# Optimization experiments

Measured on AMD Instinct MI355X. Metric: run time of the kernel, lower is better.

The kernel has to match this reference:

```python
import jax, jax.numpy as jnp
import numpy as np

# MiniCPM3 MLA attention dims
HIDDEN = 2560
N_HEADS = 40
Q_LORA = 768
KV_LORA = 256
ROPE_D = 32
NOPE_D = 64
V_D = HIDDEN // N_HEADS          # 64
Q_HEAD_D = NOPE_D + ROPE_D       # 96
ROPE_BASE = 10000.0
EPS = 1e-6


def setup_inputs() -> dict:
    key = jax.random.key(0)
    ks = jax.random.split(key, 8)
    B, S = 1, 2048
    sc = lambda fan_in: 1.0 / np.sqrt(fan_in)
    return {
        "hidden_states": jax.random.normal(ks[0], (B, S, HIDDEN), jnp.float32),
        "position_ids": jnp.arange(B * S, dtype=jnp.int64).reshape(B, S) % S,
        "w_qa": jax.random.normal(ks[1], (HIDDEN, Q_LORA), jnp.float32) * sc(HIDDEN),
        "q_a_ln_w": jnp.ones((Q_LORA,), jnp.float32),
        "w_qb": jax.random.normal(ks[2], (Q_LORA, N_HEADS * Q_HEAD_D), jnp.float32) * sc(Q_LORA),
        "w_kva": jax.random.normal(ks[3], (HIDDEN, KV_LORA + ROPE_D), jnp.float32) * sc(HIDDEN),
        "kv_a_ln_w": jnp.ones((KV_LORA,), jnp.float32),
        "w_kvb": jax.random.normal(ks[4], (KV_LORA, N_HEADS * (NOPE_D + V_D)), jnp.float32) * sc(KV_LORA),
        "w_o": jax.random.normal(ks[5], (N_HEADS * V_D, HIDDEN), jnp.float32) * sc(N_HEADS * V_D),
    }


def _rmsnorm(x, w, eps=EPS):
    var = jnp.mean(x * x, axis=-1, keepdims=True)
    return x * jax.lax.rsqrt(var + eps) * w


def _rotate_half(x):
    h = x.shape[-1] // 2
    return jnp.concatenate([-x[..., h:], x[..., :h]], axis=-1)


def _rope_cache(seq_len, dim, base, dtype=jnp.float32):
    inv_freq = 1.0 / (base ** (jnp.arange(0, dim, 2, dtype=jnp.float32) / dim))
    t = jnp.arange(seq_len, dtype=jnp.float32)
    freqs = jnp.outer(t, inv_freq)                      # [S, dim/2]
    emb = jnp.concatenate([freqs, freqs], axis=-1)      # [S, dim]
    return jnp.cos(emb).astype(dtype), jnp.sin(emb).astype(dtype)


def reference(hidden_states, position_ids, w_qa, q_a_ln_w, w_qb, w_kva, kv_a_ln_w, w_kvb, w_o):
    B, S, _ = hidden_states.shape
    # --- low-rank Q projection: a -> RMSNorm -> b ---
    q = _rmsnorm(hidden_states @ w_qa, q_a_ln_w) @ w_qb          # [B,S,H*96]
    q = q.reshape(B, S, N_HEADS, Q_HEAD_D).transpose(0, 2, 1, 3)  # [B,H,S,96]
    q_nope, q_pe = q[..., :NOPE_D], q[..., NOPE_D:]
    # --- compressed KV + shared rope key ---
    ckv = hidden_states @ w_kva                                   # [B,S,256+32]
    compressed_kv, k_pe = ckv[..., :KV_LORA], ckv[..., KV_LORA:]
    k_pe = k_pe[:, None, :, :]                                    # [B,1,S,32]
    kv = _rmsnorm(compressed_kv, kv_a_ln_w) @ w_kvb               # [B,S,H*(64+64)]
    kv = kv.reshape(B, S, N_HEADS, NOPE_D + V_D).transpose(0, 2, 1, 3)
    k_nope, v = kv[..., :NOPE_D], kv[..., NOPE_D:]                # [B,H,S,64] each
    # --- RoPE on the 32-dim rope sub-dimension (fp32, as original) ---
    cos, sin = _rope_cache(S, ROPE_D, ROPE_BASE)
    cos = cos[position_ids][:, None, :, :]                        # [B,1,S,32]
    sin = sin[position_ids][:, None, :, :]
    q_pe = q_pe * cos + _rotate_half(q_pe) * sin
    k_pe = k_pe * cos + _rotate_half(k_pe) * sin
    # --- concat nope/rope parts ---
    q_full = jnp.concatenate([q_nope, q_pe], axis=-1)             # [B,H,S,96]
    k_full = jnp.concatenate([k_nope, jnp.broadcast_to(k_pe, (B, N_HEADS, S, ROPE_D))], axis=-1)
    # --- causal SDPA with scale q_head_dim**-0.5 ---
    scale = Q_HEAD_D ** -0.5
    scores = jnp.einsum("bhqd,bhkd->bhqk", q_full, k_full) * scale
    causal = jnp.tril(jnp.ones((S, S), bool))
    scores = jnp.where(causal, scores, jnp.finfo(scores.dtype).min)
    probs = jax.nn.softmax(scores, axis=-1)
    attn = jnp.einsum("bhqk,bhkd->bhqd", probs, v)                # [B,H,S,64]
    attn = attn.transpose(0, 2, 1, 3).reshape(B, S, N_HEADS * V_D)
    return attn @ w_o
```

## Files before the change

kernel.cpp:

```cpp
#include <hip/hip_runtime.h>
#include <hip/hip_bf16.h>

typedef __hip_bfloat16 bf16;
typedef __attribute__((ext_vector_type(8))) __bf16 bf16x8;
typedef __attribute__((ext_vector_type(4))) __bf16 bf16x4;
typedef __attribute__((ext_vector_type(4))) float f32x4;

constexpr int S_LEN = 2048;
constexpr int HID   = 2560;
constexpr int NH    = 40;
constexpr int QL    = 768;
constexpr int KVL   = 256;
constexpr int RD    = 32;
constexpr int ND    = 64;
constexpr int VD    = 64;
constexpr int QHD   = 96;
constexpr int QB_N  = NH * QHD;
constexpr int KVB_N = NH * (ND + VD);
constexpr int CKV_N = KVL + RD;
constexpr int AB_N  = QL + CKV_N;

#define MFMA16(a, b, c) __builtin_amdgcn_mfma_f32_16x16x32_bf16((a), (b), (c), 0, 0, 0)

__device__ __forceinline__ int get_pos(const int* pos, int s) {
  bool is64 = (pos[1] == 0 && pos[2] == 1);
  return is64 ? pos[2 * s] : pos[s];
}


__global__ void cast_f32_bf16(const float* __restrict__ src, bf16* __restrict__ dst, int n4) {
  int i = blockIdx.x * blockDim.x + threadIdx.x;
  if (i >= n4) return;
  float4 v = reinterpret_cast<const float4*>(src)[i];
  struct { bf16 a, b, c, d; } pk;
  pk.a = __float2bfloat16(v.x); pk.b = __float2bfloat16(v.y);
  pk.c = __float2bfloat16(v.z); pk.d = __float2bfloat16(v.w);
  reinterpret_cast<uint2*>(dst)[i] = *reinterpret_cast<uint2*>(&pk);
}

__global__ void transpose_cast(const float* __restrict__ src, bf16* __restrict__ dst, int K, int N) {
  __shared__ float tile[32][33];
  int nb = blockIdx.x * 32, kb = blockIdx.y * 32;
  int x = threadIdx.x, y = threadIdx.y;
#pragma unroll
  for (int j = 0; j < 4; ++j) {
    int k = kb + y + j * 8, n = nb + x;
    tile[y + j * 8][x] = (k < K && n < N) ? src[(size_t)k * N + n] : 0.f;
  }
  __syncthreads();
#pragma unroll
  for (int j = 0; j < 4; ++j) {
    int n = nb + y + j * 8, k = kb + x;
    if (n < N && k < K) dst[(size_t)n * K + k] = __float2bfloat16(tile[x][y + j * 8]);
  }
}


template<bool OBF16, bool NEDGE>
__global__ __launch_bounds__(256) void gemm_bt(const bf16* __restrict__ A,
                                               const bf16* __restrict__ B,
                                               void* __restrict__ Cv,
                                               int M, int N, int K) {
  constexpr int BM = 128, BN = 128, BK = 64;
  __shared__ __bf16 ldsA[BM * BK];
  __shared__ __bf16 ldsB[BN * BK];
  const int t = threadIdx.x;
  const int l = t & 63, w = t >> 6;
  const int lr = l & 15, lk = l >> 4;
  const int wr = w >> 1, wc = w & 1;
  const int rowbase = blockIdx.y * BM;
  const int colbase = blockIdx.x * BN;

  f32x4 acc[4][4];
#pragma unroll
  for (int m = 0; m < 4; ++m)
#pragma unroll
    for (int n = 0; n < 4; ++n) acc[m][n] = f32x4{0.f, 0.f, 0.f, 0.f};

  const int kiters = K / BK;
  for (int kt = 0; kt < kiters; ++kt) {
    const int kb = kt * BK;
#pragma unroll
    for (int it = 0; it < 4; ++it) {
      const int r  = it * 32 + w * 8 + (l >> 3);
      const int c8 = ((l & 7) * 8) ^ ((r & 7) << 3);
      const bf16* ga = A + (size_t)(rowbase + r) * K + kb + c8;
      __builtin_amdgcn_global_load_lds((const __attribute__((address_space(1))) void*)ga,
          (__attribute__((address_space(3))) void*)(ldsA + it * 2048 + w * 512), 16, 0, 0);
      int nrow = colbase + r;
      if (NEDGE) nrow = (nrow < N) ? nrow : (N - 1);
      const bf16* gb = B + (size_t)nrow * K + kb + c8;
      __builtin_amdgcn_global_load_lds((const __attribute__((address_space(1))) void*)gb,
          (__attribute__((address_space(3))) void*)(ldsB + it * 2048 + w * 512), 16, 0, 0);
    }
    __syncthreads();
#pragma unroll
    for (int kk = 0; kk < 2; ++kk) {
      bf16x8 af[4], bfr[4];
#pragma unroll
      for (int m = 0; m < 4; ++m) {
        const int row = wr * 64 + m * 16 + lr;
        const int ce  = (kk * 32 + lk * 8) ^ ((row & 7) << 3);
        af[m] = *(const bf16x8*)(ldsA + row * BK + ce);
      }
#pragma unroll
      for (int n = 0; n < 4; ++n) {
        const int row = wc * 64 + n * 16 + lr;
        const int ce  = (kk * 32 + lk * 8) ^ ((row & 7) << 3);
        bfr[n] = *(const bf16x8*)(ldsB + row * BK + ce);
      }
#pragma unroll
      for (int m = 0; m < 4; ++m)
#pragma unroll
        for (int n = 0; n < 4; ++n)
          acc[m][n] = MFMA16(af[m], bfr[n], acc[m][n]);
    }
    __syncthreads();
  }

#pragma unroll
  for (int m = 0; m < 4; ++m)
#pragma unroll
    for (int n = 0; n < 4; ++n) {
      const int col = colbase + wc * 64 + n * 16 + lr;
      if (NEDGE && col >= N) continue;
#pragma unroll
      for (int i = 0; i < 4; ++i) {
        const int row = rowbase + wr * 64 + m * 16 + lk * 4 + i;
        if (OBF16) ((bf16*)Cv)[(size_t)row * N + col] = __float2bfloat16(acc[m][n][i]);
        else       ((float*)Cv)[(size_t)row * N + col] = acc[m][n][i];
      }
    }
}

__global__ __launch_bounds__(256) void gemm_qakva(const bf16* __restrict__ A,
                                                  const bf16* __restrict__ B,
                                                  float* __restrict__ q_out,
                                                  float* __restrict__ ckv_out) {
  constexpr int BM = 128, BK = 64, K = HID, N = AB_N;
  __shared__ __bf16 ldsA[BM * BK];
  __shared__ __bf16 ldsB[64 * BK];
  const int t = threadIdx.x;
  const int l = t & 63, w = t >> 6;
  const int lr = l & 15, lk = l >> 4;
  const int rowbase = blockIdx.y * BM;
  const int colbase = blockIdx.x * 64;

  f32x4 acc[2][4];
#pragma unroll
  for (int m = 0; m < 2; ++m)
#pragma unroll
    for (int n = 0; n < 4; ++n) acc[m][n] = f32x4{0.f, 0.f, 0.f, 0.f};

  for (int kt = 0; kt < K / BK; ++kt) {
    const int kb = kt * BK;
#pragma unroll
    for (int it = 0; it < 4; ++it) {
      const int r  = it * 32 + w * 8 + (l >> 3);
      const int c8 = ((l & 7) * 8) ^ ((r & 7) << 3);
      const bf16* ga = A + (size_t)(rowbase + r) * K + kb + c8;
      __builtin_amdgcn_global_load_lds((const __attribute__((address_space(1))) void*)ga,
          (__attribute__((address_space(3))) void*)(ldsA + it * 2048 + w * 512), 16, 0, 0);
      if (it < 2) {
        int nrow = colbase + r;
        nrow = (nrow < N) ? nrow : (N - 1);
        const bf16* gb = B + (size_t)nrow * K + kb + c8;
        __builtin_amdgcn_global_load_lds((const __attribute__((address_space(1))) void*)gb,
            (__attribute__((address_space(3))) void*)(ldsB + it * 2048 + w * 512), 16, 0, 0);
      }
    }
    __syncthreads();
#pragma unroll
    for (int kk = 0; kk < 2; ++kk) {
      bf16x8 af[2], bfr[4];
#pragma unroll
      for (int m = 0; m < 2; ++m) {
        const int row = w * 32 + m * 16 + lr;
        const int ce  = (kk * 32 + lk * 8) ^ ((row & 7) << 3);
        af[m] = *(const bf16x8*)(ldsA + row * BK + ce);
      }
#pragma unroll
      for (int n = 0; n < 4; ++n) {
        const int row = n * 16 + lr;
        const int ce  = (kk * 32 + lk * 8) ^ ((row & 7) << 3);
        bfr[n] = *(const bf16x8*)(ldsB + row * BK + ce);
      }
#pragma unroll
      for (int m = 0; m < 2; ++m)
#pragma unroll
        for (int n = 0; n < 4; ++n)
          acc[m][n] = MFMA16(af[m], bfr[n], acc[m][n]);
    }
    __syncthreads();
  }

#pragma unroll
  for (int m = 0; m < 2; ++m)
#pragma unroll
    for (int n = 0; n < 4; ++n) {
      const int col = colbase + n * 16 + lr;
#pragma unroll
      for (int i = 0; i < 4; ++i) {
        const int row = rowbase + w * 32 + m * 16 + lk * 4 + i;
        if (col < QL)       q_out[(size_t)row * QL + col] = acc[m][n][i];
        else if (col < N)   ckv_out[(size_t)row * CKV_N + (col - QL)] = acc[m][n][i];
      }
    }
}

__global__ __launch_bounds__(256) void gemm_qb_rope(const bf16* __restrict__ A,
                                                    const bf16* __restrict__ B,
                                                    const float* __restrict__ ropc,
                                                    const float* __restrict__ rops,
                                                    bf16* __restrict__ qfull) {
  constexpr int BM = 128, BN = 128, BK = 64, K = QL, N = QB_N;
  __shared__ __bf16 ldsA[BM * BK];
  __shared__ __bf16 ldsB[BN * BK];
  const int t = threadIdx.x;
  const int l = t & 63, w = t >> 6;
  const int lr = l & 15, lk = l >> 4;
  const int wr = w >> 1, wc = w & 1;
  const int rowbase = blockIdx.y * BM;
  const int colbase = blockIdx.x * BN;
  const float scale = 0.14724444f;

  f32x4 acc[4][4];
#pragma unroll
  for (int m = 0; m < 4; ++m)
#pragma unroll
    for (int n = 0; n < 4; ++n) acc[m][n] = f32x4{0.f, 0.f, 0.f, 0.f};

  for (int kt = 0; kt < K / BK; ++kt) {
    const int kb = kt * BK;
#pragma unroll
    for (int it = 0; it < 4; ++it) {
      const int r  = it * 32 + w * 8 + (l >> 3);
      const int c8 = ((l & 7) * 8) ^ ((r & 7) << 3);
      const bf16* ga = A + (size_t)(rowbase + r) * K + kb + c8;
      __builtin_amdgcn_global_load_lds((const __attribute__((address_space(1))) void*)ga,
          (__attribute__((address_space(3))) void*)(ldsA + it * 2048 + w * 512), 16, 0, 0);
      const bf16* gb = B + (size_t)(colbase + r) * K + kb + c8;
      __builtin_amdgcn_global_load_lds((const __attribute__((address_space(1))) void*)gb,
          (__attribute__((address_space(3))) void*)(ldsB + it * 2048 + w * 512), 16, 0, 0);
    }
    __syncthreads();
#pragma unroll
    for (int kk = 0; kk < 2; ++kk) {
      bf16x8 af[4], bfr[4];
#pragma unroll
      for (int m = 0; m < 4; ++m) {
        const int row = wr * 64 + m * 16 + lr;
        const int ce  = (kk * 32 + lk * 8) ^ ((row & 7) << 3);
        af[m] = *(const bf16x8*)(ldsA + row * BK + ce);
      }
#pragma unroll
      for (int n = 0; n < 4; ++n) {
        const int row = wc * 64 + n * 16 + lr;
        const int ce  = (kk * 32 + lk * 8) ^ ((row & 7) << 3);
        bfr[n] = *(const bf16x8*)(ldsB + row * BK + ce);
      }
#pragma unroll
      for (int m = 0; m < 4; ++m)
#pragma unroll
        for (int n = 0; n < 4; ++n)
          acc[m][n] = MFMA16(af[m], bfr[n], acc[m][n]);
    }
    __syncthreads();
  }

#pragma unroll
  for (int m = 0; m < 4; ++m) {
    const int rowtop = rowbase + wr * 64 + m * 16 + lk * 4;
#pragma unroll
    for (int n = 0; n < 4; ++n) {
      const int c0 = colbase + wc * 64 + n * 16;
      const int h  = c0 / 96;
      const int d0 = c0 - h * 96;
      const size_t qb_ = ((size_t)h * S_LEN + rowtop) * QHD + d0 + lr;
      if (d0 < ND) {
#pragma unroll
        for (int i = 0; i < 4; ++i)
          qfull[qb_ + (size_t)i * QHD] = __float2bfloat16(acc[m][n][i] * scale);
      } else if (d0 == ND) {
#pragma unroll
        for (int i = 0; i < 4; ++i) {
          const float c = ropc[(rowtop + i) * 16 + lr];
          const float s = rops[(rowtop + i) * 16 + lr];
          const float x0 = acc[m][n][i], x1 = acc[m][n + 1][i];
          qfull[qb_ + (size_t)i * QHD] = __float2bfloat16((x0 * c - x1 * s) * scale);
        }
      } else {
#pragma unroll
        for (int i = 0; i < 4; ++i) {
          const float c = ropc[(rowtop + i) * 16 + lr];
          const float s = rops[(rowtop + i) * 16 + lr];
          const float x1 = acc[m][n][i], x0 = acc[m][n - 1][i];
          qfull[qb_ + (size_t)i * QHD] = __float2bfloat16((x1 * c + x0 * s) * scale);
        }
      }
    }
  }
}

__global__ __launch_bounds__(256) void gemm_kvb_split(const bf16* __restrict__ A,
                                                      const bf16* __restrict__ B,
                                                      bf16* __restrict__ knope,
                                                      bf16* __restrict__ vt) {
  constexpr int BM = 128, BN = 128, BK = 64, K = KVL;
  __shared__ __bf16 ldsA[BM * BK];
  __shared__ __bf16 ldsB[BN * BK];
  const int t = threadIdx.x;
  const int l = t & 63, w = t >> 6;
  const int lr = l & 15, lk = l >> 4;
  const int wr = w >> 1, wc = w & 1;
  const int rowbase = blockIdx.y * BM;
  const int h = blockIdx.x;
  const int colbase = h * BN;

  f32x4 acc[4][4];
#pragma unroll
  for (int m = 0; m < 4; ++m)
#pragma unroll
    for (int n = 0; n < 4; ++n) acc[m][n] = f32x4{0.f, 0.f, 0.f, 0.f};

  for (int kt = 0; kt < K / BK; ++kt) {
    const int kb = kt * BK;
#pragma unroll
    for (int it = 0; it < 4; ++it) {
      const int r  = it * 32 + w * 8 + (l >> 3);
      const int c8 = ((l & 7) * 8) ^ ((r & 7) << 3);
      const bf16* ga = A + (size_t)(rowbase + r) * K + kb + c8;
      __builtin_amdgcn_global_load_lds((const __attribute__((address_space(1))) void*)ga,
          (__attribute__((address_space(3))) void*)(ldsA + it * 2048 + w * 512), 16, 0, 0);
      const bf16* gb = B + (size_t)(colbase + r) * K + kb + c8;
      __builtin_amdgcn_global_load_lds((const __attribute__((address_space(1))) void*)gb,
          (__attribute__((address_space(3))) void*)(ldsB + it * 2048 + w * 512), 16, 0, 0);
    }
    __syncthreads();
#pragma unroll
    for (int kk = 0; kk < 2; ++kk) {
      bf16x8 af[4], bfr[4];
#pragma unroll
      for (int m = 0; m < 4; ++m) {
        const int row = wr * 64 + m * 16 + lr;
        const int ce  = (kk * 32 + lk * 8) ^ ((row & 7) << 3);
        af[m] = *(const bf16x8*)(ldsA + row * BK + ce);
      }
#pragma unroll
      for (int n = 0; n < 4; ++n) {
        const int row = wc * 64 + n * 16 + lr;
        const int ce  = (kk * 32 + lk * 8) ^ ((row & 7) << 3);
        bfr[n] = *(const bf16x8*)(ldsB + row * BK + ce);
      }
#pragma unroll
      for (int m = 0; m < 4; ++m)
#pragma unroll
        for (int n = 0; n < 4; ++n)
          acc[m][n] = MFMA16(af[m], bfr[n], acc[m][n]);
    }
    __syncthreads();
  }

#pragma unroll
  for (int m = 0; m < 4; ++m) {
    const int rowtop = rowbase + wr * 64 + m * 16 + lk * 4;
    if (wc == 0) {
#pragma unroll
      for (int n = 0; n < 4; ++n) {
        const int d = n * 16 + lr;
#pragma unroll
        for (int i = 0; i < 4; ++i)
          knope[((size_t)h * S_LEN + rowtop + i) * ND + d] = __float2bfloat16(acc[m][n][i]);
      }
    } else {
#pragma unroll
      for (int n = 0; n < 4; ++n) {
        const int d = n * 16 + lr;
        bf16x4 pk;
#pragma unroll
        for (int i = 0; i < 4; ++i) pk[i] = (__bf16)acc[m][n][i];
        *(bf16x4*)(vt + ((size_t)h * VD + d) * S_LEN + rowtop) = pk;
      }
    }
  }
}


__global__ void rmsnorm_rows(const float* __restrict__ in, const float* __restrict__ w,
                             bf16* __restrict__ out, int C) {
  const int r = blockIdx.x;
  const float* row = in + (size_t)r * C;
  float ss = 0.f;
  for (int c = threadIdx.x; c < C; c += 256) { float v = row[c]; ss += v * v; }
#pragma unroll
  for (int d = 32; d > 0; d >>= 1) ss += __shfl_xor(ss, d);
  __shared__ float red[4];
  if ((threadIdx.x & 63) == 0) red[threadIdx.x >> 6] = ss;
  __syncthreads();
  const float tot = red[0] + red[1] + red[2] + red[3];
  const float rs = rsqrtf(tot / (float)C + 1e-6f);
  for (int c = threadIdx.x; c < C; c += 256)
    out[(size_t)r * C + c] = __float2bfloat16(row[c] * rs * w[c]);
}

__global__ void kv_prep(const float* __restrict__ ckv, const float* __restrict__ w,
                        const int* __restrict__ pos, bf16* __restrict__ ckv_bf,
                        bf16* __restrict__ kpe, float* __restrict__ ropc,
                        float* __restrict__ rops) {
  const int s = blockIdx.x, t = threadIdx.x;
  const float* row = ckv + (size_t)s * CKV_N;
  float v[4]; float ss = 0.f;
#pragma unroll
  for (int j = 0; j < 4; ++j) { v[j] = row[t + 64 * j]; ss += v[j] * v[j]; }
#pragma unroll
  for (int d = 32; d > 0; d >>= 1) ss += __shfl_xor(ss, d);
  const float rs = rsqrtf(ss / (float)KVL + 1e-6f);
#pragma unroll
  for (int j = 0; j < 4; ++j)
    ckv_bf[(size_t)s * KVL + t + 64 * j] = __float2bfloat16(v[j] * rs * w[t + 64 * j]);
  if (t < 16) {
    const float x0 = row[KVL + t], x1 = row[KVL + 16 + t];
    const float p = (float)get_pos(pos, s);
    const float invf = exp2f(-(float)t * (13.2877124f / 16.f));
    const float ang = p * invf, c = cosf(ang), sn = sinf(ang);
    ropc[s * 16 + t] = c;
    rops[s * 16 + t] = sn;
    kpe[(size_t)s * RD + t]      = __float2bfloat16(x0 * c - x1 * sn);
    kpe[(size_t)s * RD + 16 + t] = __float2bfloat16(x1 * c + x0 * sn);
  }
}

__global__ __launch_bounds__(64) void attn_kernel(const bf16* __restrict__ qfull,
                                                  const bf16* __restrict__ knope,
                                                  const bf16* __restrict__ kpe,
                                                  const bf16* __restrict__ vt,
                                                  bf16* __restrict__ ctx) {
  const int h = blockIdx.x;
  const int qw = ((int)gridDim.y - 1 - (int)blockIdx.y) * 32;
  const int l = threadIdx.x;
  const int lr = l & 15, lk = l >> 4;
  const bf16* Q  = qfull + (size_t)h * S_LEN * QHD;
  const bf16* Kn = knope + (size_t)h * S_LEN * ND;
  const bf16* V  = vt + (size_t)h * VD * S_LEN;
  __shared__ __bf16 plds[32][64];

  bf16x8 qf[2][3];
#pragma unroll
  for (int qg = 0; qg < 2; ++qg)
#pragma unroll
    for (int ks = 0; ks < 3; ++ks)
      qf[qg][ks] = *(const bf16x8*)(Q + (size_t)(qw + qg * 16 + lr) * QHD + ks * 32 + lk * 8);

  f32x4 o[2][4];
  float mrow[2], lrow[2];
#pragma unroll
  for (int qg = 0; qg < 2; ++qg) {
#pragma unroll
    for (int dt = 0; dt < 4; ++dt) o[qg][dt] = f32x4{0.f, 0.f, 0.f, 0.f};
    mrow[qg] = -1e30f; lrow[qg] = 0.f;
  }

  bf16x8 kf[4][3];
#pragma unroll
  for (int sub = 0; sub < 4; ++sub) {
#pragma unroll
    for (int ks = 0; ks < 2; ++ks)
      kf[sub][ks] = *(const bf16x8*)(Kn + (size_t)(sub * 16 + lr) * ND + ks * 32 + lk * 8);
    kf[sub][2] = *(const bf16x8*)(kpe + (size_t)(sub * 16 + lr) * RD + lk * 8);
  }

  for (int kb = 0;; kb += 64) {
    f32x4 st[2][4];
#pragma unroll
    for (int qg = 0; qg < 2; ++qg)
#pragma unroll
      for (int sub = 0; sub < 4; ++sub) st[qg][sub] = f32x4{0.f, 0.f, 0.f, 0.f};
#pragma unroll
    for (int qg = 0; qg < 2; ++qg)
#pragma unroll
      for (int sub = 0; sub < 4; ++sub)
#pragma unroll
        for (int ks = 0; ks < 3; ++ks)
          st[qg][sub] = MFMA16(kf[sub][ks], qf[qg][ks], st[qg][sub]);

    const int nkb = kb + 64;
    if (nkb <= qw) {
#pragma unroll
      for (int sub = 0; sub < 4; ++sub) {
#pragma unroll
        for (int ks = 0; ks < 2; ++ks)
          kf[sub][ks] = *(const bf16x8*)(Kn + (size_t)(nkb + sub * 16 + lr) * ND + ks * 32 + lk * 8);
        kf[sub][2] = *(const bf16x8*)(kpe + (size_t)(nkb + sub * 16 + lr) * RD + lk * 8);
      }
    }

    const bool diag = (kb + 64 > qw);
    float tm[2];
#pragma unroll
    for (int qg = 0; qg < 2; ++qg) {
      const int q = qw + qg * 16 + lr;
      if (diag) {
#pragma unroll
        for (int sub = 0; sub < 4; ++sub)
#pragma unroll
          for (int i = 0; i < 4; ++i)
            if (kb + sub * 16 + lk * 4 + i > q) st[qg][sub][i] = -1e30f;
      }
      float m0 = -1e30f;
#pragma unroll
      for (int sub = 0; sub < 4; ++sub)
#pragma unroll
        for (int i = 0; i < 4; ++i) m0 = fmaxf(m0, st[qg][sub][i]);
      m0 = fmaxf(m0, __shfl_xor(m0, 16));
      m0 = fmaxf(m0, __shfl_xor(m0, 32));
      tm[qg] = m0;
    }

    const bool noresc = __all((tm[0] <= mrow[0] + 8.f) && (tm[1] <= mrow[1] + 8.f));
    float fac[2];
#pragma unroll
    for (int qg = 0; qg < 2; ++qg) {
      const float mnew = noresc ? mrow[qg] : fmaxf(mrow[qg], tm[qg]);
      float ts = 0.f;
#pragma unroll
      for (int sub = 0; sub < 4; ++sub) {
        bf16x4 pk;
#pragma unroll
        for (int i = 0; i < 4; ++i) {
          const float p = exp2f(st[qg][sub][i] - mnew);
          ts += p;
          pk[i] = (__bf16)p;
        }
        const int swc = (sub * 16 + lk * 4) ^ ((lr & 7) << 3);
        *(bf16x4*)(&plds[qg * 16 + lr][swc]) = pk;
      }
      ts += __shfl_xor(ts, 16);
      ts += __shfl_xor(ts, 32);
      if (noresc) {
        lrow[qg] += ts;
      } else {
        fac[qg] = exp2f(mrow[qg] - mnew);
        lrow[qg] = lrow[qg] * fac[qg] + ts;
        mrow[qg] = mnew;
      }
    }
    if (!noresc) {
#pragma unroll
      for (int qg = 0; qg < 2; ++qg)
#pragma unroll
        for (int i = 0; i < 4; ++i) {
          const float fr = __shfl(fac[qg], lk * 4 + i);
#pragma unroll
          for (int dt = 0; dt < 4; ++dt) o[qg][dt][i] *= fr;
        }
    }

#pragma unroll
    for (int h2 = 0; h2 < 2; ++h2) {
      const int swc = (h2 * 32 + lk * 8) ^ ((lr & 7) << 3);
      bf16x8 pa0 = *(const bf16x8*)(&plds[lr][swc]);
      bf16x8 pa1 = *(const bf16x8*)(&plds[16 + lr][swc]);
#pragma unroll
      for (int dt = 0; dt < 4; ++dt) {
        bf16x8 vf = *(const bf16x8*)(V + (size_t)(dt * 16 + lr) * S_LEN + kb + h2 * 32 + lk * 8);
        o[0][dt] = MFMA16(pa0, vf, o[0][dt]);
        o[1][dt] = MFMA16(pa1, vf, o[1][dt]);
      }
    }
    if (nkb > qw) break;
  }

#pragma unroll
  for (int qg = 0; qg < 2; ++qg) {
    const float linv = 1.0f / lrow[qg];
#pragma unroll
    for (int i = 0; i < 4; ++i) {
      const float inv = __shfl(linv, lk * 4 + i);
#pragma unroll
      for (int dt = 0; dt < 4; ++dt) {
        const int row = qw + qg * 16 + lk * 4 + i;
        const int col = h * VD + dt * 16 + lr;
        ctx[(size_t)row * HID + col] = __float2bfloat16(o[qg][dt][i] * inv);
      }
    }
  }
}


extern "C" void kernel_launch(void* const* d_in, const int* in_sizes, int n_in,
                              void* d_out, int out_size, void* d_ws, size_t ws_size,
                              hipStream_t stream) {
  const float* hidden = (const float*)d_in[0];
  const int*   pos    = (const int*)d_in[1];
  const float* w_qa   = (const float*)d_in[2];
  const float* q_ln   = (const float*)d_in[3];
  const float* w_qb   = (const float*)d_in[4];
  const float* w_kva  = (const float*)d_in[5];
  const float* kv_ln  = (const float*)d_in[6];
  const float* w_kvb  = (const float*)d_in[7];
  const float* w_o    = (const float*)d_in[8];
  float* out = (float*)d_out;
  char* ws = (char*)d_ws;
  (void)in_sizes; (void)n_in; (void)out_size; (void)ws_size;

  size_t off = 0;
  auto take = [&](size_t bytes) -> char* {
    char* p = ws + off;
    off = (off + bytes + 255) & ~(size_t)255;
    return p;
  };
  bf16*  hid_bf = (bf16*)take((size_t)S_LEN * HID * 2);
  bf16*  wabT   = (bf16*)take((size_t)AB_N * HID * 2);
  bf16*  wqbT   = (bf16*)take((size_t)QB_N * QL * 2);
  bf16*  wkvbT  = (bf16*)take((size_t)KVB_N * KVL * 2);
  bf16*  woT    = (bf16*)take((size_t)HID * HID * 2);
  float* qlora  = (float*)take((size_t)S_LEN * QL * 4);
  bf16*  qa_bf  = (bf16*)take((size_t)S_LEN * QL * 2);
  bf16*  qfull  = (bf16*)take((size_t)NH * S_LEN * QHD * 2);
  float* ckv    = (float*)take((size_t)S_LEN * CKV_N * 4);
  bf16*  ckv_bf = (bf16*)take((size_t)S_LEN * KVL * 2);
  bf16*  kpe    = (bf16*)take((size_t)S_LEN * RD * 2);
  float* ropc   = (float*)take((size_t)S_LEN * 16 * 4);
  float* rops   = (float*)take((size_t)S_LEN * 16 * 4);
  bf16*  knope  = (bf16*)take((size_t)NH * S_LEN * ND * 2);
  bf16*  vt     = (bf16*)take((size_t)NH * VD * S_LEN * 2);
  bf16*  ctx    = (bf16*)take((size_t)S_LEN * HID * 2);

  const dim3 tb(32, 8);
  cast_f32_bf16<<<(S_LEN * HID / 4 + 255) / 256, 256, 0, stream>>>(hidden, hid_bf, S_LEN * HID / 4);
  transpose_cast<<<dim3((QL + 31) / 32, (HID + 31) / 32), tb, 0, stream>>>(w_qa, wabT, HID, QL);
  transpose_cast<<<dim3((CKV_N + 31) / 32, (HID + 31) / 32), tb, 0, stream>>>(w_kva, wabT + (size_t)QL * HID, HID, CKV_N);
  transpose_cast<<<dim3((QB_N + 31) / 32, (QL + 31) / 32), tb, 0, stream>>>(w_qb, wqbT, QL, QB_N);
  transpose_cast<<<dim3((KVB_N + 31) / 32, (KVL + 31) / 32), tb, 0, stream>>>(w_kvb, wkvbT, KVL, KVB_N);
  transpose_cast<<<dim3((HID + 31) / 32, (HID + 31) / 32), tb, 0, stream>>>(w_o, woT, HID, HID);

  gemm_qakva<<<dim3((AB_N + 63) / 64, S_LEN / 128), 256, 0, stream>>>(hid_bf, wabT, qlora, ckv);

  kv_prep<<<S_LEN, 64, 0, stream>>>(ckv, kv_ln, pos, ckv_bf, kpe, ropc, rops);

  rmsnorm_rows<<<S_LEN, 256, 0, stream>>>(qlora, q_ln, qa_bf, QL);
  gemm_qb_rope<<<dim3(QB_N / 128, S_LEN / 128), 256, 0, stream>>>(qa_bf, wqbT, ropc, rops, qfull);

  gemm_kvb_split<<<dim3(KVB_N / 128, S_LEN / 128), 256, 0, stream>>>(ckv_bf, wkvbT, knope, vt);

  attn_kernel<<<dim3(NH, S_LEN / 32), 64, 0, stream>>>(qfull, knope, kpe, vt, ctx);
  gemm_bt<false, false><<<dim3(HID / 128, S_LEN / 128), 256, 0, stream>>>(ctx, woT, out, S_LEN, HID, HID);
}
```

Before: 267.3 us.

## Compute softmax row sums via MFMA and use narrower output-projection GEMM tiles

The attention kernel drops the per-row exp-sum reductions and cross-lane shuffles. It accumulates the softmax denominator with an extra MFMA against a vector of ones, using the same bf16 probabilities that feed the PV product, and restructures the diagonal-block masking and loop exit around a precomputed last key block. The output projection switches from 128x128 tiles to 128x64 tiles, doubling the grid to 640 blocks to fill more CUs. The trade-offs are extra MFMA work per key block, some bf16 rounding in the denominator, and reloading A twice as often in the output GEMM.

```diff
diff --git a/kernel.cpp b/kernel.cpp
--- a/kernel.cpp
+++ b/kernel.cpp
@@ -56,83 +56,6 @@
 }
 
 
-template<bool OBF16, bool NEDGE>
-__global__ __launch_bounds__(256) void gemm_bt(const bf16* __restrict__ A,
-                                               const bf16* __restrict__ B,
-                                               void* __restrict__ Cv,
-                                               int M, int N, int K) {
-  constexpr int BM = 128, BN = 128, BK = 64;
-  __shared__ __bf16 ldsA[BM * BK];
-  __shared__ __bf16 ldsB[BN * BK];
-  const int t = threadIdx.x;
-  const int l = t & 63, w = t >> 6;
-  const int lr = l & 15, lk = l >> 4;
-  const int wr = w >> 1, wc = w & 1;
-  const int rowbase = blockIdx.y * BM;
-  const int colbase = blockIdx.x * BN;
-
-  f32x4 acc[4][4];
-#pragma unroll
-  for (int m = 0; m < 4; ++m)
-#pragma unroll
-    for (int n = 0; n < 4; ++n) acc[m][n] = f32x4{0.f, 0.f, 0.f, 0.f};
-
-  const int kiters = K / BK;
-  for (int kt = 0; kt < kiters; ++kt) {
-    const int kb = kt * BK;
-#pragma unroll
-    for (int it = 0; it < 4; ++it) {
-      const int r  = it * 32 + w * 8 + (l >> 3);
-      const int c8 = ((l & 7) * 8) ^ ((r & 7) << 3);
-      const bf16* ga = A + (size_t)(rowbase + r) * K + kb + c8;
-      __builtin_amdgcn_global_load_lds((const __attribute__((address_space(1))) void*)ga,
-          (__attribute__((address_space(3))) void*)(ldsA + it * 2048 + w * 512), 16, 0, 0);
-      int nrow = colbase + r;
-      if (NEDGE) nrow = (nrow < N) ? nrow : (N - 1);
-      const bf16* gb = B + (size_t)nrow * K + kb + c8;
-      __builtin_amdgcn_global_load_lds((const __attribute__((address_space(1))) void*)gb,
-          (__attribute__((address_space(3))) void*)(ldsB + it * 2048 + w * 512), 16, 0, 0);
-    }
-    __syncthreads();
-#pragma unroll
-    for (int kk = 0; kk < 2; ++kk) {
-      bf16x8 af[4], bfr[4];
-#pragma unroll
-      for (int m = 0; m < 4; ++m) {
-        const int row = wr * 64 + m * 16 + lr;
-        const int ce  = (kk * 32 + lk * 8) ^ ((row & 7) << 3);
-        af[m] = *(const bf16x8*)(ldsA + row * BK + ce);
-      }
-#pragma unroll
-      for (int n = 0; n < 4; ++n) {
-        const int row = wc * 64 + n * 16 + lr;
-        const int ce  = (kk * 32 + lk * 8) ^ ((row & 7) << 3);
-        bfr[n] = *(const bf16x8*)(ldsB + row * BK + ce);
-      }
-#pragma unroll
-      for (int m = 0; m < 4; ++m)
-#pragma unroll
-        for (int n = 0; n < 4; ++n)
-          acc[m][n] = MFMA16(af[m], bfr[n], acc[m][n]);
-    }
-    __syncthreads();
-  }
-
-#pragma unroll
-  for (int m = 0; m < 4; ++m)
-#pragma unroll
-    for (int n = 0; n < 4; ++n) {
-      const int col = colbase + wc * 64 + n * 16 + lr;
-      if (NEDGE && col >= N) continue;
-#pragma unroll
-      for (int i = 0; i < 4; ++i) {
-        const int row = rowbase + wr * 64 + m * 16 + lk * 4 + i;
-        if (OBF16) ((bf16*)Cv)[(size_t)row * N + col] = __float2bfloat16(acc[m][n][i]);
-        else       ((float*)Cv)[(size_t)row * N + col] = acc[m][n][i];
-      }
-    }
-}
-
 __global__ __launch_bounds__(256) void gemm_qakva(const bf16* __restrict__ A,
                                                   const bf16* __restrict__ B,
                                                   float* __restrict__ q_out,
@@ -204,6 +127,77 @@
         const int row = rowbase + w * 32 + m * 16 + lk * 4 + i;
         if (col < QL)       q_out[(size_t)row * QL + col] = acc[m][n][i];
         else if (col < N)   ckv_out[(size_t)row * CKV_N + (col - QL)] = acc[m][n][i];
+      }
+    }
+}
+
+__global__ __launch_bounds__(256) void gemm_out64(const bf16* __restrict__ A,
+                                                  const bf16* __restrict__ B,
+                                                  float* __restrict__ C) {
+  constexpr int BM = 128, BK = 64, K = HID, N = HID;
+  __shared__ __bf16 ldsA[BM * BK];
+  __shared__ __bf16 ldsB[64 * BK];
+  const int t = threadIdx.x;
+  const int l = t & 63, w = t >> 6;
+  const int lr = l & 15, lk = l >> 4;
+  const int rowbase = blockIdx.y * BM;
+  const int colbase = blockIdx.x * 64;
+
+  f32x4 acc[2][4];
+#pragma unroll
+  for (int m = 0; m < 2; ++m)
+#pragma unroll
+    for (int n = 0; n < 4; ++n) acc[m][n] = f32x4{0.f, 0.f, 0.f, 0.f};
+
+  for (int kt = 0; kt < K / BK; ++kt) {
+    const int kb = kt * BK;
+#pragma unroll
+    for (int it = 0; it < 4; ++it) {
+      const int r  = it * 32 + w * 8 + (l >> 3);
+      const int c8 = ((l & 7) * 8) ^ ((r & 7) << 3);
+      const bf16* ga = A + (size_t)(rowbase + r) * K + kb + c8;
+      __builtin_amdgcn_global_load_lds((const __attribute__((address_space(1))) void*)ga,
+          (__attribute__((address_space(3))) void*)(ldsA + it * 2048 + w * 512), 16, 0, 0);
+      if (it < 2) {
+        const bf16* gb = B + (size_t)(colbase + r) * K + kb + c8;
+        __builtin_amdgcn_global_load_lds((const __attribute__((address_space(1))) void*)gb,
+            (__attribute__((address_space(3))) void*)(ldsB + it * 2048 + w * 512), 16, 0, 0);
+      }
+    }
+    __syncthreads();
+#pragma unroll
+    for (int kk = 0; kk < 2; ++kk) {
+      bf16x8 af[2], bfr[4];
+#pragma unroll
+      for (int m = 0; m < 2; ++m) {
+        const int row = w * 32 + m * 16 + lr;
+        const int ce  = (kk * 32 + lk * 8) ^ ((row & 7) << 3);
+        af[m] = *(const bf16x8*)(ldsA + row * BK + ce);
+      }
+#pragma unroll
+      for (int n = 0; n < 4; ++n) {
+        const int row = n * 16 + lr;
+        const int ce  = (kk * 32 + lk * 8) ^ ((row & 7) << 3);
+        bfr[n] = *(const bf16x8*)(ldsB + row * BK + ce);
+      }
+#pragma unroll
+      for (int m = 0; m < 2; ++m)
+#pragma unroll
+        for (int n = 0; n < 4; ++n)
+          acc[m][n] = MFMA16(af[m], bfr[n], acc[m][n]);
+    }
+    __syncthreads();
+  }
+
+#pragma unroll
+  for (int m = 0; m < 2; ++m)
+#pragma unroll
+    for (int n = 0; n < 4; ++n) {
+      const int col = colbase + n * 16 + lr;
+#pragma unroll
+      for (int i = 0; i < 4; ++i) {
+        const int row = rowbase + w * 32 + m * 16 + lk * 4 + i;
+        C[(size_t)row * N + col] = acc[m][n][i];
       }
     }
 }
@@ -439,6 +433,7 @@
   const int qw = ((int)gridDim.y - 1 - (int)blockIdx.y) * 32;
   const int l = threadIdx.x;
   const int lr = l & 15, lk = l >> 4;
+  const int lastkb = (qw >> 6) << 6;
   const bf16* Q  = qfull + (size_t)h * S_LEN * QHD;
   const bf16* Kn = knope + (size_t)h * S_LEN * ND;
   const bf16* V  = vt + (size_t)h * VD * S_LEN;
@@ -451,13 +446,18 @@
     for (int ks = 0; ks < 3; ++ks)
       qf[qg][ks] = *(const bf16x8*)(Q + (size_t)(qw + qg * 16 + lr) * QHD + ks * 32 + lk * 8);
 
-  f32x4 o[2][4];
-  float mrow[2], lrow[2];
+  bf16x8 ones;
+#pragma unroll
+  for (int c = 0; c < 8; ++c) ones[c] = (__bf16)1.0f;
+
+  f32x4 o[2][4], lac[2];
+  float mrow[2];
 #pragma unroll
   for (int qg = 0; qg < 2; ++qg) {
 #pragma unroll
     for (int dt = 0; dt < 4; ++dt) o[qg][dt] = f32x4{0.f, 0.f, 0.f, 0.f};
-    mrow[qg] = -1e30f; lrow[qg] = 0.f;
+    lac[qg] = f32x4{0.f, 0.f, 0.f, 0.f};
+    mrow[qg] = -1e30f;
   }
 
   bf16x8 kf[4][3];
@@ -484,7 +484,7 @@
           st[qg][sub] = MFMA16(kf[sub][ks], qf[qg][ks], st[qg][sub]);
 
     const int nkb = kb + 64;
-    if (nkb <= qw) {
+    if (nkb <= lastkb) {
 #pragma unroll
       for (int sub = 0; sub < 4; ++sub) {
 #pragma unroll
@@ -494,65 +494,55 @@
       }
     }
 
-    const bool diag = (kb + 64 > qw);
+    if (kb == lastkb) {
+#pragma unroll
+      for (int qg = 0; qg < 2; ++qg) {
+        const int q = qw + qg * 16 + lr;
+#pragma unroll
+        for (int sub = 0; sub < 4; ++sub)
+#pragma unroll
+          for (int ii = 0; ii < 4; ++ii)
+            if (kb + sub * 16 + lk * 4 + ii > q) st[qg][sub][ii] = -1e30f;
+      }
+    }
+
     float tm[2];
 #pragma unroll
     for (int qg = 0; qg < 2; ++qg) {
-      const int q = qw + qg * 16 + lr;
-      if (diag) {
-#pragma unroll
-        for (int sub = 0; sub < 4; ++sub)
-#pragma unroll
-          for (int i = 0; i < 4; ++i)
-            if (kb + sub * 16 + lk * 4 + i > q) st[qg][sub][i] = -1e30f;
-      }
       float m0 = -1e30f;
 #pragma unroll
       for (int sub = 0; sub < 4; ++sub)
 #pragma unroll
-        for (int i = 0; i < 4; ++i) m0 = fmaxf(m0, st[qg][sub][i]);
+        for (int ii = 0; ii < 4; ++ii) m0 = fmaxf(m0, st[qg][sub][ii]);
       m0 = fmaxf(m0, __shfl_xor(m0, 16));
       m0 = fmaxf(m0, __shfl_xor(m0, 32));
       tm[qg] = m0;
     }
 
     const bool noresc = __all((tm[0] <= mrow[0] + 8.f) && (tm[1] <= mrow[1] + 8.f));
-    float fac[2];
 #pragma unroll
     for (int qg = 0; qg < 2; ++qg) {
       const float mnew = noresc ? mrow[qg] : fmaxf(mrow[qg], tm[qg]);
-      float ts = 0.f;
 #pragma unroll
       for (int sub = 0; sub < 4; ++sub) {
         bf16x4 pk;
 #pragma unroll
-        for (int i = 0; i < 4; ++i) {
-          const float p = exp2f(st[qg][sub][i] - mnew);
-          ts += p;
-          pk[i] = (__bf16)p;
-        }
+        for (int ii = 0; ii < 4; ++ii)
+          pk[ii] = (__bf16)exp2f(st[qg][sub][ii] - mnew);
         const int swc = (sub * 16 + lk * 4) ^ ((lr & 7) << 3);
         *(bf16x4*)(&plds[qg * 16 + lr][swc]) = pk;
       }
-      ts += __shfl_xor(ts, 16);
-      ts += __shfl_xor(ts, 32);
-      if (noresc) {
-        lrow[qg] += ts;
-      } else {
-        fac[qg] = exp2f(mrow[qg] - mnew);
-        lrow[qg] = lrow[qg] * fac[qg] + ts;
+      if (!noresc) {
+        const float fac = exp2f(mrow[qg] - mnew);
         mrow[qg] = mnew;
-      }
-    }
-    if (!noresc) {
-#pragma unroll
-      for (int qg = 0; qg < 2; ++qg)
-#pragma unroll
-        for (int i = 0; i < 4; ++i) {
-          const float fr = __shfl(fac[qg], lk * 4 + i);
-#pragma unroll
-          for (int dt = 0; dt < 4; ++dt) o[qg][dt][i] *= fr;
+#pragma unroll
+        for (int ii = 0; ii < 4; ++ii) {
+          const float fr = __shfl(fac, lk * 4 + ii);
+#pragma unroll
+          for (int dt = 0; dt < 4; ++dt) o[qg][dt][ii] *= fr;
+          lac[qg][ii] *= fr;
         }
+      }
     }
 
 #pragma unroll
@@ -566,24 +556,23 @@
         o[0][dt] = MFMA16(pa0, vf, o[0][dt]);
         o[1][dt] = MFMA16(pa1, vf, o[1][dt]);
       }
-    }
-    if (nkb > qw) break;
-  }
-
-#pragma unroll
-  for (int qg = 0; qg < 2; ++qg) {
-    const float linv = 1.0f / lrow[qg];
-#pragma unroll
-    for (int i = 0; i < 4; ++i) {
-      const float inv = __shfl(linv, lk * 4 + i);
-#pragma unroll
-      for (int dt = 0; dt < 4; ++dt) {
-        const int row = qw + qg * 16 + lk * 4 + i;
-        const int col = h * VD + dt * 16 + lr;
-        ctx[(size_t)row * HID + col] = __float2bfloat16(o[qg][dt][i] * inv);
-      }
-    }
-  }
+      lac[0] = MFMA16(pa0, ones, lac[0]);
+      lac[1] = MFMA16(pa1, ones, lac[1]);
+    }
+    if (kb == lastkb) break;
+  }
+
+#pragma unroll
+  for (int qg = 0; qg < 2; ++qg)
+#pragma unroll
+    for (int ii = 0; ii < 4; ++ii) {
+      const float inv = 1.0f / lac[qg][ii];
+      const int row = qw + qg * 16 + lk * 4 + ii;
+#pragma unroll
+      for (int dt = 0; dt < 4; ++dt)
+        ctx[(size_t)row * HID + h * VD + dt * 16 + lr] =
+            __float2bfloat16(o[qg][dt][ii] * inv);
+    }
 }
 
 
@@ -644,5 +633,5 @@
   gemm_kvb_split<<<dim3(KVB_N / 128, S_LEN / 128), 256, 0, stream>>>(ckv_bf, wkvbT, knope, vt);
 
   attn_kernel<<<dim3(NH, S_LEN / 32), 64, 0, stream>>>(qfull, knope, kpe, vt, ctx);
-  gemm_bt<false, false><<<dim3(HID / 128, S_LEN / 128), 256, 0, stream>>>(ctx, woT, out, S_LEN, HID, HID);
-}
+  gemm_out64<<<dim3(HID / 64, S_LEN / 128), 256, 0, stream>>>(ctx, woT, out);
+}
```

Result: faster. 251.0 us (-6.1%).

## Pack K nope and rope into one per-head buffer; narrow output GEMM tiles

Applied to the files above, without the earlier changes.

The nope part of K and the rotated rope key are now written into a single per-head buffer with a 96-wide row, filled by both the kv-b GEMM and kv_prep. The attention kernel can then load each K row with one contiguous stride instead of reading two separate arrays. The output projection also switches from 128x128 tiles to 128x64 tiles, doubling the block count for better CU occupancy. In exchange, kv_prep writes the rope key 40 times per token, adding some write traffic, and each output tile reuses less data.

```diff
diff --git a/kernel.cpp b/kernel.cpp
--- a/kernel.cpp
+++ b/kernel.cpp
@@ -56,83 +56,6 @@
 }
 
 
-template<bool OBF16, bool NEDGE>
-__global__ __launch_bounds__(256) void gemm_bt(const bf16* __restrict__ A,
-                                               const bf16* __restrict__ B,
-                                               void* __restrict__ Cv,
-                                               int M, int N, int K) {
-  constexpr int BM = 128, BN = 128, BK = 64;
-  __shared__ __bf16 ldsA[BM * BK];
-  __shared__ __bf16 ldsB[BN * BK];
-  const int t = threadIdx.x;
-  const int l = t & 63, w = t >> 6;
-  const int lr = l & 15, lk = l >> 4;
-  const int wr = w >> 1, wc = w & 1;
-  const int rowbase = blockIdx.y * BM;
-  const int colbase = blockIdx.x * BN;
-
-  f32x4 acc[4][4];
-#pragma unroll
-  for (int m = 0; m < 4; ++m)
-#pragma unroll
-    for (int n = 0; n < 4; ++n) acc[m][n] = f32x4{0.f, 0.f, 0.f, 0.f};
-
-  const int kiters = K / BK;
-  for (int kt = 0; kt < kiters; ++kt) {
-    const int kb = kt * BK;
-#pragma unroll
-    for (int it = 0; it < 4; ++it) {
-      const int r  = it * 32 + w * 8 + (l >> 3);
-      const int c8 = ((l & 7) * 8) ^ ((r & 7) << 3);
-      const bf16* ga = A + (size_t)(rowbase + r) * K + kb + c8;
-      __builtin_amdgcn_global_load_lds((const __attribute__((address_space(1))) void*)ga,
-          (__attribute__((address_space(3))) void*)(ldsA + it * 2048 + w * 512), 16, 0, 0);
-      int nrow = colbase + r;
-      if (NEDGE) nrow = (nrow < N) ? nrow : (N - 1);
-      const bf16* gb = B + (size_t)nrow * K + kb + c8;
-      __builtin_amdgcn_global_load_lds((const __attribute__((address_space(1))) void*)gb,
-          (__attribute__((address_space(3))) void*)(ldsB + it * 2048 + w * 512), 16, 0, 0);
-    }
-    __syncthreads();
-#pragma unroll
-    for (int kk = 0; kk < 2; ++kk) {
-      bf16x8 af[4], bfr[4];
-#pragma unroll
-      for (int m = 0; m < 4; ++m) {
-        const int row = wr * 64 + m * 16 + lr;
-        const int ce  = (kk * 32 + lk * 8) ^ ((row & 7) << 3);
-        af[m] = *(const bf16x8*)(ldsA + row * BK + ce);
-      }
-#pragma unroll
-      for (int n = 0; n < 4; ++n) {
-        const int row = wc * 64 + n * 16 + lr;
-        const int ce  = (kk * 32 + lk * 8) ^ ((row & 7) << 3);
-        bfr[n] = *(const bf16x8*)(ldsB + row * BK + ce);
-      }
-#pragma unroll
-      for (int m = 0; m < 4; ++m)
-#pragma unroll
-        for (int n = 0; n < 4; ++n)
-          acc[m][n] = MFMA16(af[m], bfr[n], acc[m][n]);
-    }
-    __syncthreads();
-  }
-
-#pragma unroll
-  for (int m = 0; m < 4; ++m)
-#pragma unroll
-    for (int n = 0; n < 4; ++n) {
-      const int col = colbase + wc * 64 + n * 16 + lr;
-      if (NEDGE && col >= N) continue;
-#pragma unroll
-      for (int i = 0; i < 4; ++i) {
-        const int row = rowbase + wr * 64 + m * 16 + lk * 4 + i;
-        if (OBF16) ((bf16*)Cv)[(size_t)row * N + col] = __float2bfloat16(acc[m][n][i]);
-        else       ((float*)Cv)[(size_t)row * N + col] = acc[m][n][i];
-      }
-    }
-}
-
 __global__ __launch_bounds__(256) void gemm_qakva(const bf16* __restrict__ A,
                                                   const bf16* __restrict__ B,
                                                   float* __restrict__ q_out,
@@ -204,6 +127,77 @@
         const int row = rowbase + w * 32 + m * 16 + lk * 4 + i;
         if (col < QL)       q_out[(size_t)row * QL + col] = acc[m][n][i];
         else if (col < N)   ckv_out[(size_t)row * CKV_N + (col - QL)] = acc[m][n][i];
+      }
+    }
+}
+
+__global__ __launch_bounds__(256) void gemm_out64(const bf16* __restrict__ A,
+                                                  const bf16* __restrict__ B,
+                                                  float* __restrict__ C) {
+  constexpr int BM = 128, BK = 64, K = HID, N = HID;
+  __shared__ __bf16 ldsA[BM * BK];
+  __shared__ __bf16 ldsB[64 * BK];
+  const int t = threadIdx.x;
+  const int l = t & 63, w = t >> 6;
+  const int lr = l & 15, lk = l >> 4;
+  const int rowbase = blockIdx.y * BM;
+  const int colbase = blockIdx.x * 64;
+
+  f32x4 acc[2][4];
+#pragma unroll
+  for (int m = 0; m < 2; ++m)
+#pragma unroll
+    for (int n = 0; n < 4; ++n) acc[m][n] = f32x4{0.f, 0.f, 0.f, 0.f};
+
+  for (int kt = 0; kt < K / BK; ++kt) {
+    const int kb = kt * BK;
+#pragma unroll
+    for (int it = 0; it < 4; ++it) {
+      const int r  = it * 32 + w * 8 + (l >> 3);
+      const int c8 = ((l & 7) * 8) ^ ((r & 7) << 3);
+      const bf16* ga = A + (size_t)(rowbase + r) * K + kb + c8;
+      __builtin_amdgcn_global_load_lds((const __attribute__((address_space(1))) void*)ga,
+          (__attribute__((address_space(3))) void*)(ldsA + it * 2048 + w * 512), 16, 0, 0);
+      if (it < 2) {
+        const bf16* gb = B + (size_t)(colbase + r) * K + kb + c8;
+        __builtin_amdgcn_global_load_lds((const __attribute__((address_space(1))) void*)gb,
+            (__attribute__((address_space(3))) void*)(ldsB + it * 2048 + w * 512), 16, 0, 0);
+      }
+    }
+    __syncthreads();
+#pragma unroll
+    for (int kk = 0; kk < 2; ++kk) {
+      bf16x8 af[2], bfr[4];
+#pragma unroll
+      for (int m = 0; m < 2; ++m) {
+        const int row = w * 32 + m * 16 + lr;
+        const int ce  = (kk * 32 + lk * 8) ^ ((row & 7) << 3);
+        af[m] = *(const bf16x8*)(ldsA + row * BK + ce);
+      }
+#pragma unroll
+      for (int n = 0; n < 4; ++n) {
+        const int row = n * 16 + lr;
+        const int ce  = (kk * 32 + lk * 8) ^ ((row & 7) << 3);
+        bfr[n] = *(const bf16x8*)(ldsB + row * BK + ce);
+      }
+#pragma unroll
+      for (int m = 0; m < 2; ++m)
+#pragma unroll
+        for (int n = 0; n < 4; ++n)
+          acc[m][n] = MFMA16(af[m], bfr[n], acc[m][n]);
+    }
+    __syncthreads();
+  }
+
+#pragma unroll
+  for (int m = 0; m < 2; ++m)
+#pragma unroll
+    for (int n = 0; n < 4; ++n) {
+      const int col = colbase + n * 16 + lr;
+#pragma unroll
+      for (int i = 0; i < 4; ++i) {
+        const int row = rowbase + w * 32 + m * 16 + lk * 4 + i;
+        C[(size_t)row * N + col] = acc[m][n][i];
       }
     }
 }
@@ -304,7 +298,7 @@
 
 __global__ __launch_bounds__(256) void gemm_kvb_split(const bf16* __restrict__ A,
                                                       const bf16* __restrict__ B,
-                                                      bf16* __restrict__ knope,
+                                                      bf16* __restrict__ kfull,
                                                       bf16* __restrict__ vt) {
   constexpr int BM = 128, BN = 128, BK = 64, K = KVL;
   __shared__ __bf16 ldsA[BM * BK];
@@ -370,7 +364,7 @@
         const int d = n * 16 + lr;
 #pragma unroll
         for (int i = 0; i < 4; ++i)
-          knope[((size_t)h * S_LEN + rowtop + i) * ND + d] = __float2bfloat16(acc[m][n][i]);
+          kfull[((size_t)h * S_LEN + rowtop + i) * QHD + d] = __float2bfloat16(acc[m][n][i]);
       }
     } else {
 #pragma unroll
@@ -405,9 +399,10 @@
 
 __global__ void kv_prep(const float* __restrict__ ckv, const float* __restrict__ w,
                         const int* __restrict__ pos, bf16* __restrict__ ckv_bf,
-                        bf16* __restrict__ kpe, float* __restrict__ ropc,
+                        bf16* __restrict__ kfull, float* __restrict__ ropc,
                         float* __restrict__ rops) {
   const int s = blockIdx.x, t = threadIdx.x;
+  __shared__ bf16 pe_lds[32];
   const float* row = ckv + (size_t)s * CKV_N;
   float v[4]; float ss = 0.f;
 #pragma unroll
@@ -425,14 +420,18 @@
     const float ang = p * invf, c = cosf(ang), sn = sinf(ang);
     ropc[s * 16 + t] = c;
     rops[s * 16 + t] = sn;
-    kpe[(size_t)s * RD + t]      = __float2bfloat16(x0 * c - x1 * sn);
-    kpe[(size_t)s * RD + 16 + t] = __float2bfloat16(x1 * c + x0 * sn);
+    pe_lds[t]      = __float2bfloat16(x0 * c - x1 * sn);
+    pe_lds[16 + t] = __float2bfloat16(x1 * c + x0 * sn);
+  }
+  __syncthreads();
+  for (int idx = t; idx < NH * 32; idx += 64) {
+    const int h = idx >> 5, d = idx & 31;
+    kfull[((size_t)h * S_LEN + s) * QHD + ND + d] = pe_lds[d];
   }
 }
 
 __global__ __launch_bounds__(64) void attn_kernel(const bf16* __restrict__ qfull,
-                                                  const bf16* __restrict__ knope,
-                                                  const bf16* __restrict__ kpe,
+                                                  const bf16* __restrict__ kfull,
                                                   const bf16* __restrict__ vt,
                                                   bf16* __restrict__ ctx) {
   const int h = blockIdx.x;
@@ -440,7 +439,7 @@
   const int l = threadIdx.x;
   const int lr = l & 15, lk = l >> 4;
   const bf16* Q  = qfull + (size_t)h * S_LEN * QHD;
-  const bf16* Kn = knope + (size_t)h * S_LEN * ND;
+  const bf16* Kf = kfull + (size_t)h * S_LEN * QHD;
   const bf16* V  = vt + (size_t)h * VD * S_LEN;
   __shared__ __bf16 plds[32][64];
 
@@ -462,12 +461,10 @@
 
   bf16x8 kf[4][3];
 #pragma unroll
-  for (int sub = 0; sub < 4; ++sub) {
-#pragma unroll
-    for (int ks = 0; ks < 2; ++ks)
-      kf[sub][ks] = *(const bf16x8*)(Kn + (size_t)(sub * 16 + lr) * ND + ks * 32 + lk * 8);
-    kf[sub][2] = *(const bf16x8*)(kpe + (size_t)(sub * 16 + lr) * RD + lk * 8);
-  }
+  for (int sub = 0; sub < 4; ++sub)
+#pragma unroll
+    for (int ks = 0; ks < 3; ++ks)
+      kf[sub][ks] = *(const bf16x8*)(Kf + (size_t)(sub * 16 + lr) * QHD + ks * 32 + lk * 8);
 
   for (int kb = 0;; kb += 64) {
     f32x4 st[2][4];
@@ -486,12 +483,10 @@
     const int nkb = kb + 64;
     if (nkb <= qw) {
 #pragma unroll
-      for (int sub = 0; sub < 4; ++sub) {
-#pragma unroll
-        for (int ks = 0; ks < 2; ++ks)
-          kf[sub][ks] = *(const bf16x8*)(Kn + (size_t)(nkb + sub * 16 + lr) * ND + ks * 32 + lk * 8);
-        kf[sub][2] = *(const bf16x8*)(kpe + (size_t)(nkb + sub * 16 + lr) * RD + lk * 8);
-      }
+      for (int sub = 0; sub < 4; ++sub)
+#pragma unroll
+        for (int ks = 0; ks < 3; ++ks)
+          kf[sub][ks] = *(const bf16x8*)(Kf + (size_t)(nkb + sub * 16 + lr) * QHD + ks * 32 + lk * 8);
     }
 
     const bool diag = (kb + 64 > qw);
@@ -619,10 +614,9 @@
   bf16*  qfull  = (bf16*)take((size_t)NH * S_LEN * QHD * 2);
   float* ckv    = (float*)take((size_t)S_LEN * CKV_N * 4);
   bf16*  ckv_bf = (bf16*)take((size_t)S_LEN * KVL * 2);
-  bf16*  kpe    = (bf16*)take((size_t)S_LEN * RD * 2);
   float* ropc   = (float*)take((size_t)S_LEN * 16 * 4);
   float* rops   = (float*)take((size_t)S_LEN * 16 * 4);
-  bf16*  knope  = (bf16*)take((size_t)NH * S_LEN * ND * 2);
+  bf16*  kfull  = (bf16*)take((size_t)NH * S_LEN * QHD * 2);
   bf16*  vt     = (bf16*)take((size_t)NH * VD * S_LEN * 2);
   bf16*  ctx    = (bf16*)take((size_t)S_LEN * HID * 2);
 
@@ -636,13 +630,13 @@
 
   gemm_qakva<<<dim3((AB_N + 63) / 64, S_LEN / 128), 256, 0, stream>>>(hid_bf, wabT, qlora, ckv);
 
-  kv_prep<<<S_LEN, 64, 0, stream>>>(ckv, kv_ln, pos, ckv_bf, kpe, ropc, rops);
+  kv_prep<<<S_LEN, 64, 0, stream>>>(ckv, kv_ln, pos, ckv_bf, kfull, ropc, rops);
 
   rmsnorm_rows<<<S_LEN, 256, 0, stream>>>(qlora, q_ln, qa_bf, QL);
   gemm_qb_rope<<<dim3(QB_N / 128, S_LEN / 128), 256, 0, stream>>>(qa_bf, wqbT, ropc, rops, qfull);
 
-  gemm_kvb_split<<<dim3(KVB_N / 128, S_LEN / 128), 256, 0, stream>>>(ckv_bf, wkvbT, knope, vt);
-
-  attn_kernel<<<dim3(NH, S_LEN / 32), 64, 0, stream>>>(qfull, knope, kpe, vt, ctx);
-  gemm_bt<false, false><<<dim3(HID / 128, S_LEN / 128), 256, 0, stream>>>(ctx, woT, out, S_LEN, HID, HID);
-}
+  gemm_kvb_split<<<dim3(KVB_N / 128, S_LEN / 128), 256, 0, stream>>>(ckv_bf, wkvbT, kfull, vt);
+
+  attn_kernel<<<dim3(NH, S_LEN / 32), 64, 0, stream>>>(qfull, kfull, vt, ctx);
+  gemm_out64<<<dim3(HID / 64, S_LEN / 128), 256, 0, stream>>>(ctx, woT, out);
+}
```

Result: faster. 241.9 us (-9.5%).
